# Performance work log

Measured on AMD Instinct MI355X. Metric: run time of the kernel, lower is better.

The kernel has to match this reference:

```python
import jax, jax.numpy as jnp
import numpy as np

NUM_RAYS = 131072
NUM_EXISTING = 256
NUM_SAMPLES = 96
NEAR, FAR = 2.0, 6.0


def setup_inputs() -> dict:
    key = jax.random.key(0)
    k_w, = jax.random.split(key, 1)
    weights = jax.random.uniform(k_w, (NUM_RAYS, NUM_EXISTING, 1), dtype=jnp.float32)
    # existing bins: uniform partition of [0,1] in normalized spacing coordinates
    edges = jnp.linspace(0.0, 1.0, NUM_EXISTING + 1, dtype=jnp.float32)
    spacing_starts = jnp.broadcast_to(edges[:-1, None], (NUM_RAYS, NUM_EXISTING, 1))
    spacing_ends = jnp.broadcast_to(edges[1:, None], (NUM_RAYS, NUM_EXISTING, 1))
    return {
        "weights": weights,
        "spacing_starts": spacing_starts,
        "spacing_ends": spacing_ends,
        "num_samples": NUM_SAMPLES,
    }


def _pdf_sample(weights, spacing_starts, spacing_ends, num_samples, eps=1e-5):
    num_bins = num_samples + 1  # static Python int
    w = weights[..., 0]                                   # [R, N]
    w_sum = jnp.sum(w, axis=-1, keepdims=True)            # [R, 1]
    padding = jax.nn.relu(eps - w_sum)
    w = w + padding / w.shape[-1]
    w_sum = w_sum + padding
    pdf = w / w_sum
    cdf = jnp.minimum(jnp.ones_like(pdf), jnp.cumsum(pdf, axis=-1))
    cdf = jnp.concatenate([jnp.zeros_like(cdf[..., :1]), cdf], axis=-1)  # [R, N+1]

    # eval path: deterministic bin midpoints in CDF space
    u = jnp.linspace(0.0, 1.0 - 1.0 / num_bins, num_bins, dtype=cdf.dtype)
    u = u + 1.0 / (2 * num_bins)
    u = jnp.broadcast_to(u, (*cdf.shape[:-1], num_bins))   # [R, num_bins]

    existing_bins = jnp.concatenate(
        [spacing_starts[..., 0], spacing_ends[..., -1:, 0]], axis=-1
    )                                                       # [R, N+1]

    # per-ray binary search (right bisection), vmapped over rays
    inds = jax.vmap(lambda c, uu: jnp.searchsorted(c, uu, side="right"))(cdf, u)
    last = existing_bins.shape[-1] - 1
    below = jnp.clip(inds - 1, 0, last)
    above = jnp.clip(inds, 0, last)

    cdf_g0 = jnp.take_along_axis(cdf, below, axis=-1)
    bins_g0 = jnp.take_along_axis(existing_bins, below, axis=-1)
    cdf_g1 = jnp.take_along_axis(cdf, above, axis=-1)
    bins_g1 = jnp.take_along_axis(existing_bins, above, axis=-1)

    denom = cdf_g1 - cdf_g0
    denom = jnp.where(denom < 1e-5, jnp.ones_like(denom), denom)
    t = jnp.clip((u - cdf_g0) / denom, 0.0, 1.0)
    bins = bins_g0 + t * (bins_g1 - bins_g0)
    bins = jax.lax.stop_gradient(bins)  # .detach() in original

    euclidean_bins = NEAR + bins * (FAR - NEAR)  # spacing_to_euclidean_fn (linear)
    # stack [euclidean_bins, spacing_bins]: [2, R, num_bins]
    return jnp.stack([euclidean_bins, bins], axis=0)


def reference(weights, spacing_starts, spacing_ends, num_samples):
    return _pdf_sample(weights, spacing_starts, spacing_ends, num_samples)
```

## Files before the change

### kernel.cpp

```cpp
#include <hip/hip_runtime.h>


#define NUM_RAYS 131072
#define NUM_EXISTING 256
#define NUM_BINS 97
#define EPS_W 1e-5f

constexpr int WAVES_PER_BLOCK = 4;
constexpr int BLOCK = 64 * WAVES_PER_BLOCK;
constexpr int ROW  = NUM_EXISTING + 4;
constexpr int CROW = NUM_EXISTING;
constexpr int DROW = 128;

template<int CTRL, int RMASK>
__device__ __forceinline__ float scan_add(float v) {
    int t = __builtin_amdgcn_update_dpp(0, __float_as_int(v), CTRL, RMASK, 0xF, true);
    return v + __int_as_float(t);
}

__global__ __launch_bounds__(BLOCK) void pdf_sample_kernel(
    const float* __restrict__ weights,
    const float* __restrict__ spacing_starts,
    const float* __restrict__ spacing_ends,
    float* __restrict__ out)
{
    __shared__ __align__(16) float s_bin[WAVES_PER_BLOCK][ROW];
    __shared__ __align__(16) float s_cdf[WAVES_PER_BLOCK][CROW];
    __shared__ __align__(16) int   s_dn[WAVES_PER_BLOCK][DROW];

    const int wave = threadIdx.x >> 6;
    const int lane = threadIdx.x & 63;
    const int ray  = blockIdx.x * WAVES_PER_BLOCK + wave;

    const float* wrow = weights        + (size_t)ray * NUM_EXISTING;
    const float* srow = spacing_starts + (size_t)ray * NUM_EXISTING;

    float4 w4 = reinterpret_cast<const float4*>(wrow)[lane];
    float4 b4 = reinterpret_cast<const float4*>(srow)[lane];

    float* binw = s_bin[wave];
    float* cdfw = s_cdf[wave];
    int*   dnw  = s_dn[wave];

    reinterpret_cast<float4*>(binw)[lane] = b4;
    if (lane == 0)
        binw[NUM_EXISTING] = spacing_ends[(size_t)ray * NUM_EXISTING + NUM_EXISTING - 1];

    dnw[lane]      = 0;
    dnw[lane + 64] = 0;

    float sl = (w4.x + w4.y) + (w4.z + w4.w);
    float v = sl;
    v = scan_add<0x111, 0xF>(v);
    v = scan_add<0x112, 0xF>(v);
    v = scan_add<0x114, 0xF>(v);
    v = scan_add<0x118, 0xF>(v);
    v = scan_add<0x142, 0xA>(v);
    v = scan_add<0x143, 0xC>(v);
    float incl  = v;
    float total = __int_as_float(__builtin_amdgcn_readlane(__float_as_int(v), 63));
    float excl  = incl - sl;

    float padding = fmaxf(EPS_W - total, 0.0f);
    float inv     = __builtin_amdgcn_rcpf(total + padding);
    float padinv  = padding * inv * (1.0f / (float)NUM_EXISTING);

    float base = fmaf(excl, inv, (float)(4 * lane) * padinv);
    float cc = base;
    cc = fmaf(w4.x, inv, cc + padinv); float c0 = fminf(cc, 1.0f);
    cc = fmaf(w4.y, inv, cc + padinv); float c1 = fminf(cc, 1.0f);
    cc = fmaf(w4.z, inv, cc + padinv); float c2 = fminf(cc, 1.0f);
    cc = fmaf(w4.w, inv, cc + padinv); float c3 = fminf(cc, 1.0f);

    reinterpret_cast<float4*>(cdfw)[lane] = make_float4(c0, c1, c2, c3);

    int m0 = (int)ceilf(fmaf(97.0f, c0, -0.5f));
    int m1 = (int)ceilf(fmaf(97.0f, c1, -0.5f));
    int m2 = (int)ceilf(fmaf(97.0f, c2, -0.5f));
    int m3 = (int)ceilf(fmaf(97.0f, c3, -0.5f));

    int mn = __shfl_down(m0, 1);
    mn = (lane == 63) ? NUM_BINS : mn;

    int bb3 = min(m3, mn);
    int bb2 = min(m2, bb3);
    int bb1 = min(m1, bb2);
    int bb0 = min(m0, bb1);

    int e1 = 4 * lane + 1;
    for (int j = bb0; j < bb1; ++j) dnw[j] = e1;
    for (int j = bb1; j < bb2; ++j) dnw[j] = e1 + 1;
    for (int j = bb2; j < bb3; ++j) dnw[j] = e1 + 2;
    for (int j = bb3; j < mn;  ++j) dnw[j] = e1 + 3;

    int2 bl2 = *reinterpret_cast<const int2*>(&dnw[2 * lane]);

    float* out_e = out + (size_t)ray * NUM_BINS;
    float* out_s = out + (size_t)NUM_RAYS * NUM_BINS + (size_t)ray * NUM_BINS;

    constexpr float U_STEP = 1.0f / (float)NUM_BINS;
    constexpr float U_HALF = 0.5f / (float)NUM_BINS;

    #pragma unroll
    for (int k = 0; k < 2; ++k) {
        int j = 2 * lane + k;
        if (j < NUM_BINS) {
            int below = k ? bl2.y : bl2.x;
            below = below > 255 ? 255 : below;
            int cb = below - 1; cb = cb < 0 ? 0 : cb;

            float u = fmaf((float)j, U_STEP, U_HALF);

            float x   = cdfw[cb];
            float cg1 = cdfw[below];
            float cg0 = (below == 0) ? 0.0f : x;

            float bg0 = binw[below];
            float bg1 = binw[below + 1];

            float denom = cg1 - cg0;
            denom = (denom < 1e-5f) ? 1.0f : denom;
            float t = (u - cg0) * __builtin_amdgcn_rcpf(denom);
            t = fminf(fmaxf(t, 0.0f), 1.0f);

            float bins = fmaf(t, bg1 - bg0, bg0);

            out_e[j] = fmaf(bins, 4.0f, 2.0f);
            out_s[j] = bins;
        }
    }
}

extern "C" void kernel_launch(void* const* d_in, const int* in_sizes, int n_in,
                              void* d_out, int out_size, void* d_ws, size_t ws_size,
                              hipStream_t stream) {
    const float* weights        = (const float*)d_in[0];
    const float* spacing_starts = (const float*)d_in[1];
    const float* spacing_ends   = (const float*)d_in[2];
    float* out = (float*)d_out;

    dim3 grid(NUM_RAYS / WAVES_PER_BLOCK);
    dim3 block(BLOCK);
    pdf_sample_kernel<<<grid, block, 0, stream>>>(weights, spacing_starts, spacing_ends, out);
}
```

Measured before the change: 351.2 us.

## Emit samples directly per CDF interval instead of LDS scatter-gather search

The kernel no longer uses shared memory. Each lane takes the output bins whose midpoints fall inside its own four CDF intervals and writes those samples directly. Neighbour CDF values, bin counts and bin edges come from wave-level DPP shifts instead of an LDS index table followed by a gather. This removes LDS writes and reads and the scatter loop, at the cost of less regular, lane-divergent global stores and a rare fallback loop for intervals that cover several outputs.

```diff
diff --git a/kernel.cpp b/kernel.cpp
--- a/kernel.cpp
+++ b/kernel.cpp
@@ -8,14 +8,57 @@
 
 constexpr int WAVES_PER_BLOCK = 4;
 constexpr int BLOCK = 64 * WAVES_PER_BLOCK;
-constexpr int ROW  = NUM_EXISTING + 4;
-constexpr int CROW = NUM_EXISTING;
-constexpr int DROW = 128;
+constexpr float U_STEP = 1.0f / (float)NUM_BINS;
+constexpr float U_HALF = 0.5f / (float)NUM_BINS;
 
 template<int CTRL, int RMASK>
 __device__ __forceinline__ float scan_add(float v) {
     int t = __builtin_amdgcn_update_dpp(0, __float_as_int(v), CTRL, RMASK, 0xF, true);
     return v + __int_as_float(t);
+}
+__device__ __forceinline__ int shfl_up1_i(int v) {
+    return __builtin_amdgcn_update_dpp(0, v, 0x138, 0xF, 0xF, true);
+}
+__device__ __forceinline__ float shfl_up1_f(float v) {
+    return __int_as_float(shfl_up1_i(__float_as_int(v)));
+}
+__device__ __forceinline__ float shfl_dn1_f(float v) {
+    return __int_as_float(__builtin_amdgcn_update_dpp(0, __float_as_int(v), 0x130, 0xF, 0xF, true));
+}
+
+__device__ __forceinline__ void emit1(int lo, int hi, float cg0, float cg1,
+                                      float bg0, float bg1,
+                                      float* __restrict__ out_e,
+                                      float* __restrict__ out_s)
+{
+    if (lo < hi) {
+        float denom = cg1 - cg0;
+        denom = (denom < 1e-5f) ? 1.0f : denom;
+        float u = fmaf((float)lo, U_STEP, U_HALF);
+        float t = (u - cg0) * __builtin_amdgcn_rcpf(denom);
+        t = fminf(fmaxf(t, 0.0f), 1.0f);
+        float bins = fmaf(t, bg1 - bg0, bg0);
+        out_e[lo] = fmaf(bins, 4.0f, 2.0f);
+        out_s[lo] = bins;
+    }
+}
+
+__device__ __forceinline__ void emit_loop(int lo, int hi, float cg0, float cg1,
+                                          float bg0, float bg1,
+                                          float* __restrict__ out_e,
+                                          float* __restrict__ out_s)
+{
+    float denom = cg1 - cg0;
+    denom = (denom < 1e-5f) ? 1.0f : denom;
+    float rd = __builtin_amdgcn_rcpf(denom);
+    float bd = bg1 - bg0;
+    for (int j = lo; j < hi; ++j) {
+        float u = fmaf((float)j, U_STEP, U_HALF);
+        float t = fminf(fmaxf((u - cg0) * rd, 0.0f), 1.0f);
+        float bins = fmaf(t, bd, bg0);
+        out_e[j] = fmaf(bins, 4.0f, 2.0f);
+        out_s[j] = bins;
+    }
 }
 
 __global__ __launch_bounds__(BLOCK) void pdf_sample_kernel(
@@ -24,30 +67,13 @@
     const float* __restrict__ spacing_ends,
     float* __restrict__ out)
 {
-    __shared__ __align__(16) float s_bin[WAVES_PER_BLOCK][ROW];
-    __shared__ __align__(16) float s_cdf[WAVES_PER_BLOCK][CROW];
-    __shared__ __align__(16) int   s_dn[WAVES_PER_BLOCK][DROW];
-
     const int wave = threadIdx.x >> 6;
     const int lane = threadIdx.x & 63;
     const int ray  = blockIdx.x * WAVES_PER_BLOCK + wave;
 
-    const float* wrow = weights        + (size_t)ray * NUM_EXISTING;
-    const float* srow = spacing_starts + (size_t)ray * NUM_EXISTING;
-
-    float4 w4 = reinterpret_cast<const float4*>(wrow)[lane];
-    float4 b4 = reinterpret_cast<const float4*>(srow)[lane];
-
-    float* binw = s_bin[wave];
-    float* cdfw = s_cdf[wave];
-    int*   dnw  = s_dn[wave];
-
-    reinterpret_cast<float4*>(binw)[lane] = b4;
-    if (lane == 0)
-        binw[NUM_EXISTING] = spacing_ends[(size_t)ray * NUM_EXISTING + NUM_EXISTING - 1];
-
-    dnw[lane]      = 0;
-    dnw[lane + 64] = 0;
+    const float4 w4 = reinterpret_cast<const float4*>(weights        + (size_t)ray * NUM_EXISTING)[lane];
+    const float4 b4 = reinterpret_cast<const float4*>(spacing_starts + (size_t)ray * NUM_EXISTING)[lane];
+    const float bend = spacing_ends[(size_t)ray * NUM_EXISTING + (NUM_EXISTING - 1)];
 
     float sl = (w4.x + w4.y) + (w4.z + w4.w);
     float v = sl;
@@ -57,77 +83,47 @@
     v = scan_add<0x118, 0xF>(v);
     v = scan_add<0x142, 0xA>(v);
     v = scan_add<0x143, 0xC>(v);
-    float incl  = v;
     float total = __int_as_float(__builtin_amdgcn_readlane(__float_as_int(v), 63));
-    float excl  = incl - sl;
+    float excl  = v - sl;
 
     float padding = fmaxf(EPS_W - total, 0.0f);
     float inv     = __builtin_amdgcn_rcpf(total + padding);
     float padinv  = padding * inv * (1.0f / (float)NUM_EXISTING);
 
-    float base = fmaf(excl, inv, (float)(4 * lane) * padinv);
-    float cc = base;
+    float cc = fmaf(excl, inv, (float)(4 * lane) * padinv);
     cc = fmaf(w4.x, inv, cc + padinv); float c0 = fminf(cc, 1.0f);
     cc = fmaf(w4.y, inv, cc + padinv); float c1 = fminf(cc, 1.0f);
     cc = fmaf(w4.z, inv, cc + padinv); float c2 = fminf(cc, 1.0f);
     cc = fmaf(w4.w, inv, cc + padinv); float c3 = fminf(cc, 1.0f);
-
-    reinterpret_cast<float4*>(cdfw)[lane] = make_float4(c0, c1, c2, c3);
 
     int m0 = (int)ceilf(fmaf(97.0f, c0, -0.5f));
     int m1 = (int)ceilf(fmaf(97.0f, c1, -0.5f));
     int m2 = (int)ceilf(fmaf(97.0f, c2, -0.5f));
     int m3 = (int)ceilf(fmaf(97.0f, c3, -0.5f));
 
-    int mn = __shfl_down(m0, 1);
-    mn = (lane == 63) ? NUM_BINS : mn;
+    int   s0   = shfl_up1_i(m3);
+    float clo  = shfl_up1_f(c3);
+    float bhi3 = shfl_dn1_f(b4.x);
+    if (lane == 63) bhi3 = bend;
 
-    int bb3 = min(m3, mn);
-    int bb2 = min(m2, bb3);
-    int bb1 = min(m1, bb2);
-    int bb0 = min(m0, bb1);
-
-    int e1 = 4 * lane + 1;
-    for (int j = bb0; j < bb1; ++j) dnw[j] = e1;
-    for (int j = bb1; j < bb2; ++j) dnw[j] = e1 + 1;
-    for (int j = bb2; j < bb3; ++j) dnw[j] = e1 + 2;
-    for (int j = bb3; j < mn;  ++j) dnw[j] = e1 + 3;
-
-    int2 bl2 = *reinterpret_cast<const int2*>(&dnw[2 * lane]);
+    int e0 = max(m0, s0);
+    int e1 = max(m1, e0);
+    int e2 = max(m2, e1);
+    int e3 = max(m3, e2);
 
     float* out_e = out + (size_t)ray * NUM_BINS;
-    float* out_s = out + (size_t)NUM_RAYS * NUM_BINS + (size_t)ray * NUM_BINS;
+    float* out_s = out_e + (size_t)NUM_RAYS * NUM_BINS;
 
-    constexpr float U_STEP = 1.0f / (float)NUM_BINS;
-    constexpr float U_HALF = 0.5f / (float)NUM_BINS;
+    emit1(s0, e0, clo, c0, b4.x, b4.y, out_e, out_s);
+    emit1(e0, e1, c0,  c1, b4.y, b4.z, out_e, out_s);
+    emit1(e1, e2, c1,  c2, b4.z, b4.w, out_e, out_s);
+    emit1(e2, e3, c2,  c3, b4.w, bhi3, out_e, out_s);
 
-    #pragma unroll
-    for (int k = 0; k < 2; ++k) {
-        int j = 2 * lane + k;
-        if (j < NUM_BINS) {
-            int below = k ? bl2.y : bl2.x;
-            below = below > 255 ? 255 : below;
-            int cb = below - 1; cb = cb < 0 ? 0 : cb;
-
-            float u = fmaf((float)j, U_STEP, U_HALF);
-
-            float x   = cdfw[cb];
-            float cg1 = cdfw[below];
-            float cg0 = (below == 0) ? 0.0f : x;
-
-            float bg0 = binw[below];
-            float bg1 = binw[below + 1];
-
-            float denom = cg1 - cg0;
-            denom = (denom < 1e-5f) ? 1.0f : denom;
-            float t = (u - cg0) * __builtin_amdgcn_rcpf(denom);
-            t = fminf(fmaxf(t, 0.0f), 1.0f);
-
-            float bins = fmaf(t, bg1 - bg0, bg0);
-
-            out_e[j] = fmaf(bins, 4.0f, 2.0f);
-            out_s[j] = bins;
-        }
+    if ((((e0 - s0) | (e1 - e0)) | ((e2 - e1) | (e3 - e2))) > 1) {
+        emit_loop(s0 + 1, e0, clo, c0, b4.x, b4.y, out_e, out_s);
+        emit_loop(e0 + 1, e1, c0,  c1, b4.y, b4.z, out_e, out_s);
+        emit_loop(e1 + 1, e2, c1,  c2, b4.z, b4.w, out_e, out_s);
+        emit_loop(e2 + 1, e3, c2,  c3, b4.w, bhi3, out_e, out_s);
     }
 }
 
```

Result: no change. 356.0 us (+1.4%).
